# Optimization experiments

Measured on AMD Instinct MI355X. Metric: run time of the kernel, lower is better.

## Reference

```python
import jax, jax.numpy as jnp
import numpy as np

DIM = 512
NUM_HEADS = 8


def setup_inputs() -> dict:
    key = jax.random.key(0)
    ks = jax.random.split(key, 9)
    B, C, H, W = 8, DIM, 32, 32
    s = 1.0 / np.sqrt(DIM)  # conv-style init scale
    return {
        "x": jax.random.normal(ks[0], (B, C, H, W), jnp.float32),
        "Wq": jax.random.normal(ks[1], (DIM, DIM), jnp.float32) * s,
        "bq": jnp.zeros((DIM,), jnp.float32),
        "Wk": jax.random.normal(ks[2], (DIM, DIM), jnp.float32) * s,
        "bk": jnp.zeros((DIM,), jnp.float32),
        "Wv": jax.random.normal(ks[3], (DIM, DIM), jnp.float32) * s,
        "bv": jnp.zeros((DIM,), jnp.float32),
        "Wo": jax.random.normal(ks[4], (DIM, DIM), jnp.float32) * s,
        "bo": jnp.zeros((DIM,), jnp.float32),
    }


def _proj(x, W, b):
    # 1x1 conv == per-pixel linear over channels: [out_c, in_c] x [b, in_c, h, w]
    return jnp.einsum('oc,bchw->bohw', W, x) + b[None, :, None, None]


def reference(x, Wq, bq, Wk, bk, Wv, bv, Wo, bo):
    b, c, h, w = x.shape
    g = NUM_HEADS
    dh = c // g  # per-head channels
    q = _proj(x, Wq, bq)
    k = _proj(x, Wk, bk)
    v = _proj(x, Wv, bv)
    # 'b (g c) h w -> (b g) c (h w)'
    def split_heads(t):
        return t.reshape(b, g, dh, h * w).reshape(b * g, dh, h * w)
    q, k, v = split_heads(q), split_heads(k), split_heads(v)
    # note: scale uses full dim (as in the source), not per-head dim
    a = jnp.einsum('bcs,bct->bst', q, k) / jnp.sqrt(jnp.float32(c))
    a = jax.nn.softmax(a, axis=-1)  # dropout is identity at inference
    o = jnp.einsum('bst,bct->bcs', a, v)  # [(b g), dh, s]
    o = o.reshape(b, g * dh, h, w)  # '(b g) c (h w) -> b (g c) h w'
    return x + _proj(o, Wo, bo)
```

## Files before the change

### kernel.cpp

```cpp
#include <hip/hip_runtime.h>

typedef unsigned short u16;
typedef __attribute__((ext_vector_type(8))) short short8;
typedef __attribute__((ext_vector_type(4))) short sh4;
typedef __attribute__((ext_vector_type(2))) int int2v;
typedef __attribute__((ext_vector_type(4))) float floatx4;

__device__ __forceinline__ float b2f(u16 u) {
  unsigned int x = ((unsigned int)u) << 16;
  return __builtin_bit_cast(float, x);
}
__device__ __forceinline__ u16 f2b(float f) {
  unsigned int x = __builtin_bit_cast(unsigned int, f);
  unsigned int r = (x + 0x7FFFu + ((x >> 16) & 1u)) >> 16;
  return (u16)r;
}
__device__ __forceinline__ unsigned int pk2bf(float a, float b) {
  unsigned int ua = __builtin_bit_cast(unsigned int, a) + 0x8000u;
  unsigned int ub = __builtin_bit_cast(unsigned int, b) + 0x8000u;
  return __builtin_amdgcn_perm(ub, ua, 0x07060302u);
}

#if __has_builtin(__builtin_amdgcn_mfma_f32_16x16x16bf16_1k)
#define MFMA16(a, b, c) __builtin_amdgcn_mfma_f32_16x16x16bf16_1k((a), (b), (c), 0, 0, 0)
#define MFMA16_DRAIN()
#else
__device__ __forceinline__ floatx4 mfma16_fb(sh4 a, sh4 b, floatx4 c) {
  asm volatile("s_nop 1\n\tv_mfma_f32_16x16x16_bf16 %0, %1, %2, %0"
               : "+v"(c) : "v"(a), "v"(b));
  return c;
}
#define MFMA16(a, b, c) mfma16_fb((a), (b), (c))
#define MFMA16_DRAIN() asm volatile("s_nop 7\n\ts_nop 7\n\ts_nop 7")
#endif

#if __has_builtin(__builtin_amdgcn_exp2f)
#define EXP2F(x) __builtin_amdgcn_exp2f(x)
#else
#define EXP2F(x) __expf((x) * 0.6931471805599453f)
#endif

#define MFMA32(a, b, c) __builtin_amdgcn_mfma_f32_16x16x32_bf16((a), (b), (c), 0, 0, 0)

#define GLL16(g, l) __builtin_amdgcn_global_load_lds(                         \
    (const __attribute__((address_space(1))) unsigned int*)(g),               \
    (__attribute__((address_space(3))) unsigned int*)(l), 16, 0, 0)

#define SC_LOG2E 0.06375872f

__device__ __forceinline__ int detect_fp32(const u16* __restrict__ x) {
  __shared__ int cnt;
  if (threadIdx.x == 0) cnt = 0;
  __syncthreads();
  int c = 0;
  if (threadIdx.x < 256) {
#pragma unroll
    for (int i = 0; i < 16; ++i) {
      u16 u = x[threadIdx.x * 16 + i];
      if (((u >> 7) & 0xFF) >= 0xC8) c++;
    }
  }
  if (c) atomicAdd(&cnt, c);
  __syncthreads();
  return cnt > 32;
}

__global__ __launch_bounds__(256) void prep(
    const u16* __restrict__ x,
    const u16* w0, const u16* w1, const u16* w2, const u16* w3,
    const u16* c0, const u16* c1, const u16* c2, const u16* c3,
    u16* __restrict__ xT, u16* __restrict__ Wc, u16* __restrict__ bc, int b0) {
  const int fp32 = detect_fp32(x);
  const int tid = threadIdx.x;
  if (blockIdx.y < 8) {
    __shared__ u16 t[64][65];
    const int lb = blockIdx.z, b = b0 + lb;
    const int p0 = blockIdx.x * 64, cc0 = blockIdx.y * 64;
    const int tx = tid & 63, ty = tid >> 6;
    if (fp32) {
      const float* xb = (const float*)x + (long)b * 524288;
#pragma unroll
      for (int i = 0; i < 16; ++i) {
        int c = ty + i * 4;
        t[c][tx] = f2b(xb[(long)(cc0 + c) * 1024 + p0 + tx]);
      }
    } else {
      const u16* xb = x + (long)b * 524288;
#pragma unroll
      for (int i = 0; i < 16; ++i) {
        int c = ty + i * 4;
        t[c][tx] = xb[(long)(cc0 + c) * 1024 + p0 + tx];
      }
    }
    __syncthreads();
    u16* xTb = xT + (long)lb * 524288;
#pragma unroll
    for (int i = 0; i < 16; ++i) {
      int p = ty + i * 4;
      xTb[(long)(p0 + p) * 512 + cc0 + tx] = t[tx][p];
    }
  } else {
    const u16* srcs[8] = {w0, w1, w2, w3, c0, c1, c2, c3};
    const int nthreads = gridDim.z * 16 * 256;
    const int flat = (blockIdx.z * 16 + blockIdx.x) * 256 + tid;
    for (int vi = flat; vi < 131072; vi += nthreads) {
      int w = vi >> 15;
      int off = (vi & 32767) * 8;
      u16* dst = Wc + w * 262144 + off;
      if (fp32) {
        const float* s = (const float*)srcs[w] + off;
        u16 tmp[8];
#pragma unroll
        for (int r = 0; r < 8; ++r) tmp[r] = f2b(s[r]);
        *(int4*)dst = *(const int4*)tmp;
      } else {
        *(int4*)dst = *(const int4*)(srcs[w] + off);
      }
    }
    for (int gi = flat; gi < 2048; gi += nthreads) {
      int t2 = gi >> 9;
      bc[gi] = fp32 ? f2b(((const float*)srcs[4 + t2])[gi & 511]) : srcs[4 + t2][gi & 511];
    }
  }
}

struct GemmLds {
  u16 As[128][32];
  u16 Bs[128][32];
};

__device__ __forceinline__ void gemm_core(const u16* __restrict__ A, int lda,
                                          const u16* __restrict__ B, int ldb,
                                          int m0, int n0, int K,
                                          GemmLds& lds, floatx4 (&acc)[4][4]) {
  const int tid = threadIdx.x;
  const int wave = tid >> 6, lane = tid & 63;
  const int quad = lane >> 4, l15 = lane & 15;
  const int wm = (wave >> 1) * 64, wn = (wave & 1) * 64;
  const int lrow = lane >> 2, lcol = (lane & 3) * 8;
  for (int k0 = 0; k0 < K; k0 += 32) {
    __syncthreads();
#pragma unroll
    for (int it = 0; it < 2; ++it) {
      const int rbase = wave * 32 + it * 16;
      GLL16(A + (long)(m0 + rbase + lrow) * lda + k0 + lcol, &lds.As[rbase][0]);
      GLL16(B + (long)(n0 + rbase + lrow) * ldb + k0 + lcol, &lds.Bs[rbase][0]);
    }
    __syncthreads();
    short8 af[4], bf[4];
#pragma unroll
    for (int i = 0; i < 4; ++i)
      af[i] = *(const short8*)&lds.As[wm + i * 16 + l15][quad * 8];
#pragma unroll
    for (int j = 0; j < 4; ++j)
      bf[j] = *(const short8*)&lds.Bs[wn + j * 16 + l15][quad * 8];
#pragma unroll
    for (int i = 0; i < 4; ++i)
#pragma unroll
      for (int j = 0; j < 4; ++j)
        acc[i][j] = MFMA32(af[i], bf[j], acc[i][j]);
  }
}

__global__ __launch_bounds__(256) void gemm_qkv(
    const u16* __restrict__ xT, const u16* __restrict__ Wc,
    const u16* __restrict__ bc, u16* __restrict__ Qt, u16* __restrict__ Kt,
    u16* __restrict__ Vv) {
  __shared__ GemmLds lds;
  const long bz = blockIdx.y;
  const u16* xb = xT + bz * 524288;
  const int bx = blockIdx.x;
  const int qk = bx < 64;
  const int t = qk ? bx : bx - 64;
  const int m0 = (t >> 3) * 128, n0 = (t & 7) * 128;
  const u16* A = qk ? xb : (Wc + 524288);
  const u16* B = qk ? Wc : xb;
  floatx4 acc[4][4] = {};
  gemm_core(A, 512, B, 512, m0, n0, 512, lds, acc);
  const int lane = threadIdx.x & 63, wave = threadIdx.x >> 6;
  const int quad = lane >> 4, l15 = lane & 15;
  const int wm = (wave >> 1) * 64, wn = (wave & 1) * 64;
  if (qk) {
    u16* Qz = Qt + bz * 524288;
    u16* Kz = Kt + bz * 524288;
#pragma unroll
    for (int i = 0; i < 4; ++i)
#pragma unroll
      for (int j = 0; j < 4; ++j)
#pragma unroll
        for (int r = 0; r < 4; ++r) {
          int gm = m0 + wm + i * 16 + quad * 4 + r;
          int gn = n0 + wn + j * 16 + l15;
          float v = acc[i][j][r] + b2f(bc[gn]);
          if (gn < 512) Qz[(long)gm * 512 + gn] = f2b(v * SC_LOG2E);
          else Kz[(long)gm * 512 + gn - 512] = f2b(v);
        }
  } else {
    u16* Vz = Vv + bz * 524288;
    const u16* bv = bc + 1024;
#pragma unroll
    for (int i = 0; i < 4; ++i)
#pragma unroll
      for (int j = 0; j < 4; ++j)
#pragma unroll
        for (int r = 0; r < 4; ++r) {
          int gm = m0 + wm + i * 16 + quad * 4 + r;
          int gn = n0 + wn + j * 16 + l15;
          float v = acc[i][j][r] + b2f(bv[gm]);
          Vz[(long)gm * 1024 + gn] = f2b(v);
        }
  }
}

__global__ __launch_bounds__(256) void gemm_out(
    const u16* __restrict__ Wo, const u16* __restrict__ bo,
    const u16* __restrict__ Ow, const u16* __restrict__ xraw,
    u16* __restrict__ out) {
  const int fp32 = detect_fp32(xraw);
  __shared__ GemmLds lds;
  const long bz = blockIdx.z;
  const u16* B = Ow + bz * 524288;
  const int m0 = blockIdx.y * 128, n0 = blockIdx.x * 128;
  floatx4 acc[4][4] = {};
  gemm_core(Wo, 512, B, 512, m0, n0, 512, lds, acc);
  const int lane = threadIdx.x & 63, wave = threadIdx.x >> 6;
  const int quad = lane >> 4, l15 = lane & 15;
  const int wm = (wave >> 1) * 64, wn = (wave & 1) * 64;
#pragma unroll
  for (int i = 0; i < 4; ++i)
#pragma unroll
    for (int j = 0; j < 4; ++j)
#pragma unroll
      for (int r = 0; r < 4; ++r) {
        int gm = m0 + wm + i * 16 + quad * 4 + r;
        int gn = n0 + wn + j * 16 + l15;
        float v = acc[i][j][r] + b2f(bo[gm]);
        long idx = bz * 524288 + (long)gm * 1024 + gn;
        if (fp32) {
          v += ((const float*)xraw)[idx];
          ((float*)out)[idx] = v;
        } else {
          v += b2f(xraw[idx]);
          out[idx] = f2b(v);
        }
      }
}

#define AP 72
__global__ __launch_bounds__(512, 4) void attn(
    const u16* __restrict__ Qt, const u16* __restrict__ Kt,
    const u16* __restrict__ V, u16* __restrict__ O) {
  __shared__ alignas(16) u16 Ks[2][64][AP];
  __shared__ alignas(16) u16 Vs[2][64][AP];
  const int bg = blockIdx.x;
  const int lb = bg >> 3, head = bg & 7;
  const int s0 = blockIdx.y * 128;
  const int tid = threadIdx.x;
  const int wave = tid >> 6, lane = tid & 63;
  const int quad = lane >> 4, l15 = lane & 15;

  const u16* Qb = Qt + (long)lb * 524288 + head * 64;
  const u16* Kb = Kt + (long)lb * 524288 + head * 64;
  const u16* Vb = V + (long)(lb * 512 + head * 64) * 1024;
  u16* Ob = O + (long)lb * 524288 + head * 64;

  short8 bq[2];
#pragma unroll
  for (int kk = 0; kk < 2; ++kk)
    bq[kk] = *(const short8*)&Qb[(long)(s0 + wave * 16 + l15) * 512 +
                                 kk * 32 + quad * 8];

  const int r0 = tid >> 3, o0 = (tid & 7) * 8;
  int4 kreg, vreg;
  kreg = *(const int4*)&Kb[(long)r0 * 512 + o0];
  vreg = *(const int4*)&Vb[(long)r0 * 1024 + o0];
  *(int4*)&Ks[0][r0][o0] = kreg;
  *(int4*)&Vs[0][r0][o0] = vreg;

  floatx4 acc[4] = {};
  floatx4 accl = {};
  const sh4 ones = {(short)0x3F80, (short)0x3F80, (short)0x3F80, (short)0x3F80};

  for (int it16 = 0; it16 < 16; ++it16) {
    const int buf = it16 & 1;
    const int t0n = (it16 + 1) * 64;
    if (it16 < 15) {
      kreg = *(const int4*)&Kb[(long)(t0n + r0) * 512 + o0];
      vreg = *(const int4*)&Vb[(long)r0 * 1024 + t0n + o0];
    }
    __syncthreads();

    floatx4 p[4] = {};
#pragma unroll
    for (int kk = 0; kk < 2; ++kk) {
      short8 ak[4];
#pragma unroll
      for (int mi = 0; mi < 4; ++mi)
        ak[mi] = *(const short8*)&Ks[buf][mi * 16 + l15][kk * 32 + quad * 8];
#pragma unroll
      for (int mi = 0; mi < 4; ++mi)
        p[mi] = MFMA32(ak[mi], bq[kk], p[mi]);
    }

    sh4 pk[4];
#pragma unroll
    for (int mi = 0; mi < 4; ++mi) {
      float e0 = EXP2F(p[mi][0]);
      float e1 = EXP2F(p[mi][1]);
      float e2 = EXP2F(p[mi][2]);
      float e3 = EXP2F(p[mi][3]);
      int2v w;
      w.x = (int)pk2bf(e0, e1);
      w.y = (int)pk2bf(e2, e3);
      pk[mi] = __builtin_bit_cast(sh4, w);
    }

#pragma unroll
    for (int mi = 0; mi < 4; ++mi) accl = MFMA16(ones, pk[mi], accl);

#pragma unroll
    for (int mi = 0; mi < 4; ++mi) {
      sh4 av[4];
#pragma unroll
      for (int ci = 0; ci < 4; ++ci)
        av[ci] = *(const sh4*)&Vs[buf][ci * 16 + l15][mi * 16 + quad * 4];
#pragma unroll
      for (int ci = 0; ci < 4; ++ci)
        acc[ci] = MFMA16(av[ci], pk[mi], acc[ci]);
    }

    if (it16 < 15) {
      const int nb = 1 - buf;
      *(int4*)&Ks[nb][r0][o0] = kreg;
      *(int4*)&Vs[nb][r0][o0] = vreg;
    }
  }
  MFMA16_DRAIN();

  const float inv = 1.0f / accl[0];

  u16 (*Os)[AP] = (u16(*)[AP]) & Ks[0][0][0];
  __syncthreads();
#pragma unroll
  for (int ci = 0; ci < 4; ++ci) {
    int2v w;
    w.x = (int)pk2bf(acc[ci][0] * inv, acc[ci][1] * inv);
    w.y = (int)pk2bf(acc[ci][2] * inv, acc[ci][3] * inv);
    *(int2v*)&Os[wave * 16 + l15][ci * 16 + quad * 4] = w;
  }
  __syncthreads();
  {
    const int srow = tid >> 2, c16 = (tid & 3) * 16;
    *(int4*)&Ob[(long)(s0 + srow) * 512 + c16] = *(const int4*)&Os[srow][c16];
    *(int4*)&Ob[(long)(s0 + srow) * 512 + c16 + 8] = *(const int4*)&Os[srow][c16 + 8];
  }
}

extern "C" void kernel_launch(void* const* d_in, const int* in_sizes, int n_in,
                              void* d_out, int out_size, void* d_ws, size_t ws_size,
                              hipStream_t stream) {
  const u16* x  = (const u16*)d_in[0];
  const u16* Wq = (const u16*)d_in[1];
  const u16* bq = (const u16*)d_in[2];
  const u16* Wk = (const u16*)d_in[3];
  const u16* bk = (const u16*)d_in[4];
  const u16* Wv = (const u16*)d_in[5];
  const u16* bv = (const u16*)d_in[6];
  const u16* Wo = (const u16*)d_in[7];
  const u16* bo = (const u16*)d_in[8];
  u16* out = (u16*)d_out;
  u16* ws = (u16*)d_ws;

  const size_t PLAN_A_BYTES = 27267072;

  if (ws_size >= PLAN_A_BYTES) {
    u16* xT = ws;
    u16* Kt = ws + 4194304;
    u16* Vv = ws + 8388608;
    u16* Wc = ws + 12582912;
    u16* bc = ws + 13631488;
    u16* Qt = out;
    u16* Ow = xT;

    prep<<<dim3(16, 9, 8), 256, 0, stream>>>(x, Wq, Wk, Wv, Wo,
                                             bq, bk, bv, bo, xT, Wc, bc, 0);
    gemm_qkv<<<dim3(96, 8), 256, 0, stream>>>(xT, Wc, bc, Qt, Kt, Vv);
    attn<<<dim3(64, 8), 512, 0, stream>>>(Qt, Kt, Vv, Ow);
    gemm_out<<<dim3(8, 4, 8), 256, 0, stream>>>(Wc + 786432, bc + 1536, Ow, x, out);
  } else {
    u16* Ow = ws;
    u16* Kt = ws + 4194304;
    u16* Vv = ws + 6291456;
    u16* Wc = ws + 8388608;
    u16* bc = ws + 9437184;
    u16* Qt = out;

    for (int phase = 0; phase < 2; ++phase) {
      const int b0 = phase * 4;
      u16* xT = Ow + (long)phase * 2097152;
      prep<<<dim3(16, 9, 4), 256, 0, stream>>>(x, Wq, Wk, Wv, Wo,
                                               bq, bk, bv, bo, xT, Wc, bc, b0);
      gemm_qkv<<<dim3(96, 4), 256, 0, stream>>>(xT, Wc, bc, Qt, Kt, Vv);
      attn<<<dim3(32, 8), 512, 0, stream>>>(Qt, Kt, Vv, Ow + (long)b0 * 524288);
    }
    gemm_out<<<dim3(8, 4, 8), 256, 0, stream>>>(Wc + 786432, bc + 1536, Ow, x, out);
  }
}
```

Before: 177.2 us.

## Fuse prep, QKV, attention and output GEMM into one persistent kernel with grid barriers

Replaces four separate kernel launches with a single persistent kernel of 512 blocks that runs the stages back to back, separated by atomic-counter grid barriers. The GEMM tiles are reshaped to K-step 64 with 8 waves, and the output GEMM uses 128x64 tiles so each block gets one job. The aim is to remove launch overhead and per-kernel tail idle time. The grid barrier relies on all 512 blocks being co-resident, which deadlocks if occupancy is insufficient. It also drops the small-workspace fallback path.

```diff
diff --git a/kernel.cpp b/kernel.cpp
--- a/kernel.cpp
+++ b/kernel.cpp
@@ -47,6 +47,26 @@
     (__attribute__((address_space(3))) unsigned int*)(l), 16, 0, 0)
 
 #define SC_LOG2E 0.06375872f
+#define NB 512
+#define AP 72
+
+union SMem {
+  struct { u16 t[2][64][65]; } tr;
+  struct { u16 As[128][64]; u16 Bs[128][64]; } gm;
+  struct { u16 Ks[2][64][AP]; u16 Vs[2][64][AP]; } at;
+};
+
+__device__ __forceinline__ void gbar(unsigned* cnt, unsigned target) {
+  __syncthreads();
+  if (threadIdx.x == 0) {
+    __threadfence();
+    __hip_atomic_fetch_add(cnt, 1u, __ATOMIC_RELAXED, __HIP_MEMORY_SCOPE_AGENT);
+    while (__hip_atomic_load(cnt, __ATOMIC_RELAXED, __HIP_MEMORY_SCOPE_AGENT) < target)
+      __builtin_amdgcn_s_sleep(2);
+    __threadfence();
+  }
+  __syncthreads();
+}
 
 __device__ __forceinline__ int detect_fp32(const u16* __restrict__ x) {
   __shared__ int cnt;
@@ -65,47 +85,165 @@
   return cnt > 32;
 }
 
-__global__ __launch_bounds__(256) void prep(
+__device__ __forceinline__ void gemm_128x128(const u16* __restrict__ A,
+                                             const u16* __restrict__ B,
+                                             SMem& sm, floatx4 (&acc)[4][2]) {
+  const int tid = threadIdx.x;
+  const int wave = tid >> 6, lane = tid & 63;
+  const int quad = lane >> 4, l15 = lane & 15;
+  const int wm = (wave >> 2) * 64, wn = (wave & 3) * 32;
+  const int srow = lane >> 3, sseg = (lane & 7) * 8;
+  for (int k0 = 0; k0 < 512; k0 += 64) {
+    __syncthreads();
+#pragma unroll
+    for (int r = 0; r < 2; ++r) {
+      const int ch = wave + r * 8;
+      GLL16(A + (long)(ch * 8 + srow) * 512 + k0 + sseg, &sm.gm.As[ch * 8][0]);
+      GLL16(B + (long)(ch * 8 + srow) * 512 + k0 + sseg, &sm.gm.Bs[ch * 8][0]);
+    }
+    __syncthreads();
+#pragma unroll
+    for (int kk = 0; kk < 2; ++kk) {
+      short8 af[4], bf[2];
+#pragma unroll
+      for (int i = 0; i < 4; ++i)
+        af[i] = *(const short8*)&sm.gm.As[wm + i * 16 + l15][kk * 32 + quad * 8];
+#pragma unroll
+      for (int j = 0; j < 2; ++j)
+        bf[j] = *(const short8*)&sm.gm.Bs[wn + j * 16 + l15][kk * 32 + quad * 8];
+#pragma unroll
+      for (int i = 0; i < 4; ++i)
+#pragma unroll
+        for (int j = 0; j < 2; ++j)
+          acc[i][j] = MFMA32(af[i], bf[j], acc[i][j]);
+    }
+  }
+}
+
+__device__ __forceinline__ void gemm_128x64(const u16* __restrict__ A,
+                                            const u16* __restrict__ B,
+                                            SMem& sm, floatx4 (&acc)[2][2]) {
+  const int tid = threadIdx.x;
+  const int wave = tid >> 6, lane = tid & 63;
+  const int quad = lane >> 4, l15 = lane & 15;
+  const int wm = (wave >> 1) * 32, wn = (wave & 1) * 32;
+  const int srow = lane >> 3, sseg = (lane & 7) * 8;
+  for (int k0 = 0; k0 < 512; k0 += 64) {
+    __syncthreads();
+#pragma unroll
+    for (int r = 0; r < 3; ++r) {
+      const int ch = wave + r * 8;
+      if (ch < 16)
+        GLL16(A + (long)(ch * 8 + srow) * 512 + k0 + sseg, &sm.gm.As[ch * 8][0]);
+      else
+        GLL16(B + (long)((ch - 16) * 8 + srow) * 512 + k0 + sseg,
+              &sm.gm.Bs[(ch - 16) * 8][0]);
+    }
+    __syncthreads();
+#pragma unroll
+    for (int kk = 0; kk < 2; ++kk) {
+      short8 af[2], bf[2];
+#pragma unroll
+      for (int i = 0; i < 2; ++i)
+        af[i] = *(const short8*)&sm.gm.As[wm + i * 16 + l15][kk * 32 + quad * 8];
+#pragma unroll
+      for (int j = 0; j < 2; ++j)
+        bf[j] = *(const short8*)&sm.gm.Bs[wn + j * 16 + l15][kk * 32 + quad * 8];
+#pragma unroll
+      for (int i = 0; i < 2; ++i)
+#pragma unroll
+        for (int j = 0; j < 2; ++j)
+          acc[i][j] = MFMA32(af[i], bf[j], acc[i][j]);
+    }
+  }
+}
+
+__device__ __forceinline__ void qkv_job(int j, const u16* __restrict__ xT,
+                                        const u16* __restrict__ Wc,
+                                        const u16* __restrict__ bc,
+                                        u16* __restrict__ Qt, u16* __restrict__ Kt,
+                                        u16* __restrict__ Vv, SMem& sm) {
+  const int lane = threadIdx.x & 63, wave = threadIdx.x >> 6;
+  const int quad = lane >> 4, l15 = lane & 15;
+  const int wm = (wave >> 2) * 64, wn = (wave & 3) * 32;
+  floatx4 acc[4][2] = {};
+  if (j < 512) {
+    const int jm = j >> 3, jn = j & 7;
+    const int b = jm >> 3, mrow = (jm & 7) * 128;
+    gemm_128x128(xT + (long)b * 524288 + (long)mrow * 512, Wc + (long)jn * 65536,
+                 sm, acc);
+    u16* Qz = Qt + (long)b * 524288;
+    u16* Kz = Kt + (long)b * 524288;
+    const int gnb = jn * 128 + wn;
+#pragma unroll
+    for (int i = 0; i < 4; ++i)
+#pragma unroll
+      for (int j2 = 0; j2 < 2; ++j2)
+#pragma unroll
+        for (int r = 0; r < 4; ++r) {
+          int gm = mrow + wm + i * 16 + quad * 4 + r;
+          int gn = gnb + j2 * 16 + l15;
+          float v = acc[i][j2][r] + b2f(bc[gn]);
+          if (gn < 512) Qz[(long)gm * 512 + gn] = f2b(v * SC_LOG2E);
+          else Kz[(long)gm * 512 + gn - 512] = f2b(v);
+        }
+  } else {
+    const int vj = j - 512;
+    const int b = vj >> 5, t = vj & 31;
+    const int m0 = (t >> 3) * 128, n0 = (t & 7) * 128;
+    gemm_128x128(Wc + 524288 + (long)m0 * 512, xT + (long)b * 524288 + (long)n0 * 512,
+                 sm, acc);
+    u16* Vz = Vv + (long)b * 524288;
+#pragma unroll
+    for (int i = 0; i < 4; ++i)
+#pragma unroll
+      for (int j2 = 0; j2 < 2; ++j2)
+#pragma unroll
+        for (int r = 0; r < 4; ++r) {
+          int gm = m0 + wm + i * 16 + quad * 4 + r;
+          int gn = n0 + wn + j2 * 16 + l15;
+          Vz[(long)gm * 1024 + gn] = f2b(acc[i][j2][r] + b2f(bc[1024 + gm]));
+        }
+  }
+}
+
+__global__ __launch_bounds__(512, 4) void fused(
     const u16* __restrict__ x,
     const u16* w0, const u16* w1, const u16* w2, const u16* w3,
     const u16* c0, const u16* c1, const u16* c2, const u16* c3,
-    u16* __restrict__ xT, u16* __restrict__ Wc, u16* __restrict__ bc, int b0) {
+    u16* __restrict__ xT, u16* __restrict__ Kt, u16* __restrict__ Vv,
+    u16* __restrict__ Wc, u16* __restrict__ bc,
+    u16* __restrict__ Qt, u16* __restrict__ outp, unsigned* __restrict__ bar) {
+  __shared__ SMem sm;
+  const int bid = blockIdx.x, tid = threadIdx.x;
   const int fp32 = detect_fp32(x);
-  const int tid = threadIdx.x;
-  if (blockIdx.y < 8) {
-    __shared__ u16 t[64][65];
-    const int lb = blockIdx.z, b = b0 + lb;
-    const int p0 = blockIdx.x * 64, cc0 = blockIdx.y * 64;
-    const int tx = tid & 63, ty = tid >> 6;
+  u16* Ow = xT;
+
+  {
+    const int sub = tid >> 8, st = tid & 255;
+    const int tj = bid * 2 + sub;
+    const int b = tj >> 7, rem = tj & 127;
+    const int p0 = (rem >> 3) * 64, cc0 = (rem & 7) * 64;
+    const int tx = st & 63, ty = st >> 6;
     if (fp32) {
       const float* xb = (const float*)x + (long)b * 524288;
 #pragma unroll
       for (int i = 0; i < 16; ++i) {
         int c = ty + i * 4;
-        t[c][tx] = f2b(xb[(long)(cc0 + c) * 1024 + p0 + tx]);
+        sm.tr.t[sub][c][tx] = f2b(xb[(long)(cc0 + c) * 1024 + p0 + tx]);
       }
     } else {
       const u16* xb = x + (long)b * 524288;
 #pragma unroll
       for (int i = 0; i < 16; ++i) {
         int c = ty + i * 4;
-        t[c][tx] = xb[(long)(cc0 + c) * 1024 + p0 + tx];
-      }
-    }
-    __syncthreads();
-    u16* xTb = xT + (long)lb * 524288;
-#pragma unroll
-    for (int i = 0; i < 16; ++i) {
-      int p = ty + i * 4;
-      xTb[(long)(p0 + p) * 512 + cc0 + tx] = t[tx][p];
-    }
-  } else {
+        sm.tr.t[sub][c][tx] = xb[(long)(cc0 + c) * 1024 + p0 + tx];
+      }
+    }
     const u16* srcs[8] = {w0, w1, w2, w3, c0, c1, c2, c3};
-    const int nthreads = gridDim.z * 16 * 256;
-    const int flat = (blockIdx.z * 16 + blockIdx.x) * 256 + tid;
-    for (int vi = flat; vi < 131072; vi += nthreads) {
-      int w = vi >> 15;
-      int off = (vi & 32767) * 8;
+    const int flat = bid * 512 + tid;
+    if (flat < 131072) {
+      int w = flat >> 15, off = (flat & 32767) * 8;
       u16* dst = Wc + w * 262144 + off;
       if (fp32) {
         const float* s = (const float*)srcs[w] + off;
@@ -117,242 +255,153 @@
         *(int4*)dst = *(const int4*)(srcs[w] + off);
       }
     }
-    for (int gi = flat; gi < 2048; gi += nthreads) {
-      int t2 = gi >> 9;
-      bc[gi] = fp32 ? f2b(((const float*)srcs[4 + t2])[gi & 511]) : srcs[4 + t2][gi & 511];
-    }
-  }
-}
-
-struct GemmLds {
-  u16 As[128][32];
-  u16 Bs[128][32];
-};
-
-__device__ __forceinline__ void gemm_core(const u16* __restrict__ A, int lda,
-                                          const u16* __restrict__ B, int ldb,
-                                          int m0, int n0, int K,
-                                          GemmLds& lds, floatx4 (&acc)[4][4]) {
-  const int tid = threadIdx.x;
-  const int wave = tid >> 6, lane = tid & 63;
-  const int quad = lane >> 4, l15 = lane & 15;
-  const int wm = (wave >> 1) * 64, wn = (wave & 1) * 64;
-  const int lrow = lane >> 2, lcol = (lane & 3) * 8;
-  for (int k0 = 0; k0 < K; k0 += 32) {
-    __syncthreads();
-#pragma unroll
-    for (int it = 0; it < 2; ++it) {
-      const int rbase = wave * 32 + it * 16;
-      GLL16(A + (long)(m0 + rbase + lrow) * lda + k0 + lcol, &lds.As[rbase][0]);
-      GLL16(B + (long)(n0 + rbase + lrow) * ldb + k0 + lcol, &lds.Bs[rbase][0]);
-    }
-    __syncthreads();
-    short8 af[4], bf[4];
-#pragma unroll
-    for (int i = 0; i < 4; ++i)
-      af[i] = *(const short8*)&lds.As[wm + i * 16 + l15][quad * 8];
-#pragma unroll
-    for (int j = 0; j < 4; ++j)
-      bf[j] = *(const short8*)&lds.Bs[wn + j * 16 + l15][quad * 8];
-#pragma unroll
-    for (int i = 0; i < 4; ++i)
-#pragma unroll
-      for (int j = 0; j < 4; ++j)
-        acc[i][j] = MFMA32(af[i], bf[j], acc[i][j]);
-  }
-}
-
-__global__ __launch_bounds__(256) void gemm_qkv(
-    const u16* __restrict__ xT, const u16* __restrict__ Wc,
-    const u16* __restrict__ bc, u16* __restrict__ Qt, u16* __restrict__ Kt,
-    u16* __restrict__ Vv) {
-  __shared__ GemmLds lds;
-  const long bz = blockIdx.y;
-  const u16* xb = xT + bz * 524288;
-  const int bx = blockIdx.x;
-  const int qk = bx < 64;
-  const int t = qk ? bx : bx - 64;
-  const int m0 = (t >> 3) * 128, n0 = (t & 7) * 128;
-  const u16* A = qk ? xb : (Wc + 524288);
-  const u16* B = qk ? Wc : xb;
-  floatx4 acc[4][4] = {};
-  gemm_core(A, 512, B, 512, m0, n0, 512, lds, acc);
-  const int lane = threadIdx.x & 63, wave = threadIdx.x >> 6;
-  const int quad = lane >> 4, l15 = lane & 15;
-  const int wm = (wave >> 1) * 64, wn = (wave & 1) * 64;
-  if (qk) {
-    u16* Qz = Qt + bz * 524288;
-    u16* Kz = Kt + bz * 524288;
-#pragma unroll
-    for (int i = 0; i < 4; ++i)
-#pragma unroll
-      for (int j = 0; j < 4; ++j)
+    if (flat < 2048) {
+      int t2 = flat >> 9;
+      bc[flat] = fp32 ? f2b(((const float*)srcs[4 + t2])[flat & 511])
+                      : srcs[4 + t2][flat & 511];
+    }
+    __syncthreads();
+    u16* xTb = xT + (long)b * 524288;
+#pragma unroll
+    for (int i = 0; i < 16; ++i) {
+      int p = ty + i * 4;
+      xTb[(long)(p0 + p) * 512 + cc0 + tx] = sm.tr.t[sub][tx][p];
+    }
+  }
+  gbar(bar, NB);
+
+  qkv_job(bid, xT, Wc, bc, Qt, Kt, Vv, sm);
+  if (bid < 256) qkv_job(bid + 512, xT, Wc, bc, Qt, Kt, Vv, sm);
+  gbar(bar, 2 * NB);
+
+  {
+    const int bg = bid & 63, lb = bg >> 3, head = bg & 7;
+    const int s0 = (bid >> 6) * 128;
+    const int wave = tid >> 6, lane = tid & 63;
+    const int quad = lane >> 4, l15 = lane & 15;
+    const u16* Qb = Qt + (long)lb * 524288 + head * 64;
+    const u16* Kb = Kt + (long)lb * 524288 + head * 64;
+    const u16* Vb = Vv + (long)(lb * 512 + head * 64) * 1024;
+    u16* Ob = Ow + (long)lb * 524288 + head * 64;
+
+    short8 bq[2];
+#pragma unroll
+    for (int kk = 0; kk < 2; ++kk)
+      bq[kk] = *(const short8*)&Qb[(long)(s0 + wave * 16 + l15) * 512 +
+                                   kk * 32 + quad * 8];
+
+    const int r0 = tid >> 3, o0 = (tid & 7) * 8;
+    int4 kreg = *(const int4*)&Kb[(long)r0 * 512 + o0];
+    int4 vreg = *(const int4*)&Vb[(long)r0 * 1024 + o0];
+    *(int4*)&sm.at.Ks[0][r0][o0] = kreg;
+    *(int4*)&sm.at.Vs[0][r0][o0] = vreg;
+
+    floatx4 acc[4] = {};
+    floatx4 accl = {};
+    const sh4 ones = {(short)0x3F80, (short)0x3F80, (short)0x3F80, (short)0x3F80};
+
+    for (int it16 = 0; it16 < 16; ++it16) {
+      const int buf = it16 & 1;
+      const int t0n = (it16 + 1) * 64;
+      if (it16 < 15) {
+        kreg = *(const int4*)&Kb[(long)(t0n + r0) * 512 + o0];
+        vreg = *(const int4*)&Vb[(long)r0 * 1024 + t0n + o0];
+      }
+      __syncthreads();
+
+      floatx4 p[4] = {};
+#pragma unroll
+      for (int kk = 0; kk < 2; ++kk) {
+        short8 ak[4];
+#pragma unroll
+        for (int mi = 0; mi < 4; ++mi)
+          ak[mi] = *(const short8*)&sm.at.Ks[buf][mi * 16 + l15][kk * 32 + quad * 8];
+#pragma unroll
+        for (int mi = 0; mi < 4; ++mi)
+          p[mi] = MFMA32(ak[mi], bq[kk], p[mi]);
+      }
+
+      sh4 pk[4];
+#pragma unroll
+      for (int mi = 0; mi < 4; ++mi) {
+        float e0 = EXP2F(p[mi][0]);
+        float e1 = EXP2F(p[mi][1]);
+        float e2 = EXP2F(p[mi][2]);
+        float e3 = EXP2F(p[mi][3]);
+        int2v w;
+        w.x = (int)pk2bf(e0, e1);
+        w.y = (int)pk2bf(e2, e3);
+        pk[mi] = __builtin_bit_cast(sh4, w);
+      }
+
+#pragma unroll
+      for (int mi = 0; mi < 4; ++mi) accl = MFMA16(ones, pk[mi], accl);
+
+#pragma unroll
+      for (int mi = 0; mi < 4; ++mi) {
+        sh4 av[4];
+#pragma unroll
+        for (int ci = 0; ci < 4; ++ci)
+          av[ci] = *(const sh4*)&sm.at.Vs[buf][ci * 16 + l15][mi * 16 + quad * 4];
+#pragma unroll
+        for (int ci = 0; ci < 4; ++ci)
+          acc[ci] = MFMA16(av[ci], pk[mi], acc[ci]);
+      }
+
+      if (it16 < 15) {
+        const int nb = 1 - buf;
+        *(int4*)&sm.at.Ks[nb][r0][o0] = kreg;
+        *(int4*)&sm.at.Vs[nb][r0][o0] = vreg;
+      }
+    }
+    MFMA16_DRAIN();
+
+    const float inv = 1.0f / accl[0];
+    u16 (*Os)[AP] = (u16(*)[AP]) & sm.at.Ks[0][0][0];
+    __syncthreads();
+#pragma unroll
+    for (int ci = 0; ci < 4; ++ci) {
+      int2v w;
+      w.x = (int)pk2bf(acc[ci][0] * inv, acc[ci][1] * inv);
+      w.y = (int)pk2bf(acc[ci][2] * inv, acc[ci][3] * inv);
+      *(int2v*)&Os[wave * 16 + l15][ci * 16 + quad * 4] = w;
+    }
+    __syncthreads();
+    {
+      const int srow = tid >> 2, c16 = (tid & 3) * 16;
+      *(int4*)&Ob[(long)(s0 + srow) * 512 + c16] = *(const int4*)&Os[srow][c16];
+      *(int4*)&Ob[(long)(s0 + srow) * 512 + c16 + 8] = *(const int4*)&Os[srow][c16 + 8];
+    }
+  }
+  gbar(bar, 3 * NB);
+
+  {
+    const int b = bid >> 6, t = bid & 63;
+    const int m0 = (t >> 4) * 128, n0 = (t & 15) * 64;
+    floatx4 acc[2][2] = {};
+    gemm_128x64(Wc + 786432 + (long)m0 * 512, Ow + (long)b * 524288 + (long)n0 * 512,
+                sm, acc);
+    const int lane = tid & 63, wave = tid >> 6;
+    const int quad = lane >> 4, l15 = lane & 15;
+    const int wm = (wave >> 1) * 32, wn = (wave & 1) * 32;
+#pragma unroll
+    for (int i = 0; i < 2; ++i)
+#pragma unroll
+      for (int j2 = 0; j2 < 2; ++j2)
 #pragma unroll
         for (int r = 0; r < 4; ++r) {
           int gm = m0 + wm + i * 16 + quad * 4 + r;
-          int gn = n0 + wn + j * 16 + l15;
-          float v = acc[i][j][r] + b2f(bc[gn]);
-          if (gn < 512) Qz[(long)gm * 512 + gn] = f2b(v * SC_LOG2E);
-          else Kz[(long)gm * 512 + gn - 512] = f2b(v);
+          int gn = n0 + wn + j2 * 16 + l15;
+          float v = acc[i][j2][r] + b2f(bc[1536 + gm]);
+          long idx = (long)b * 524288 + (long)gm * 1024 + gn;
+          if (fp32) {
+            v += ((const float*)x)[idx];
+            ((float*)outp)[idx] = v;
+          } else {
+            v += b2f(x[idx]);
+            outp[idx] = f2b(v);
+          }
         }
-  } else {
-    u16* Vz = Vv + bz * 524288;
-    const u16* bv = bc + 1024;
-#pragma unroll
-    for (int i = 0; i < 4; ++i)
-#pragma unroll
-      for (int j = 0; j < 4; ++j)
-#pragma unroll
-        for (int r = 0; r < 4; ++r) {
-          int gm = m0 + wm + i * 16 + quad * 4 + r;
-          int gn = n0 + wn + j * 16 + l15;
-          float v = acc[i][j][r] + b2f(bv[gm]);
-          Vz[(long)gm * 1024 + gn] = f2b(v);
-        }
-  }
-}
-
-__global__ __launch_bounds__(256) void gemm_out(
-    const u16* __restrict__ Wo, const u16* __restrict__ bo,
-    const u16* __restrict__ Ow, const u16* __restrict__ xraw,
-    u16* __restrict__ out) {
-  const int fp32 = detect_fp32(xraw);
-  __shared__ GemmLds lds;
-  const long bz = blockIdx.z;
-  const u16* B = Ow + bz * 524288;
-  const int m0 = blockIdx.y * 128, n0 = blockIdx.x * 128;
-  floatx4 acc[4][4] = {};
-  gemm_core(Wo, 512, B, 512, m0, n0, 512, lds, acc);
-  const int lane = threadIdx.x & 63, wave = threadIdx.x >> 6;
-  const int quad = lane >> 4, l15 = lane & 15;
-  const int wm = (wave >> 1) * 64, wn = (wave & 1) * 64;
-#pragma unroll
-  for (int i = 0; i < 4; ++i)
-#pragma unroll
-    for (int j = 0; j < 4; ++j)
-#pragma unroll
-      for (int r = 0; r < 4; ++r) {
-        int gm = m0 + wm + i * 16 + quad * 4 + r;
-        int gn = n0 + wn + j * 16 + l15;
-        float v = acc[i][j][r] + b2f(bo[gm]);
-        long idx = bz * 524288 + (long)gm * 1024 + gn;
-        if (fp32) {
-          v += ((const float*)xraw)[idx];
-          ((float*)out)[idx] = v;
-        } else {
-          v += b2f(xraw[idx]);
-          out[idx] = f2b(v);
-        }
-      }
-}
-
-#define AP 72
-__global__ __launch_bounds__(512, 4) void attn(
-    const u16* __restrict__ Qt, const u16* __restrict__ Kt,
-    const u16* __restrict__ V, u16* __restrict__ O) {
-  __shared__ alignas(16) u16 Ks[2][64][AP];
-  __shared__ alignas(16) u16 Vs[2][64][AP];
-  const int bg = blockIdx.x;
-  const int lb = bg >> 3, head = bg & 7;
-  const int s0 = blockIdx.y * 128;
-  const int tid = threadIdx.x;
-  const int wave = tid >> 6, lane = tid & 63;
-  const int quad = lane >> 4, l15 = lane & 15;
-
-  const u16* Qb = Qt + (long)lb * 524288 + head * 64;
-  const u16* Kb = Kt + (long)lb * 524288 + head * 64;
-  const u16* Vb = V + (long)(lb * 512 + head * 64) * 1024;
-  u16* Ob = O + (long)lb * 524288 + head * 64;
-
-  short8 bq[2];
-#pragma unroll
-  for (int kk = 0; kk < 2; ++kk)
-    bq[kk] = *(const short8*)&Qb[(long)(s0 + wave * 16 + l15) * 512 +
-                                 kk * 32 + quad * 8];
-
-  const int r0 = tid >> 3, o0 = (tid & 7) * 8;
-  int4 kreg, vreg;
-  kreg = *(const int4*)&Kb[(long)r0 * 512 + o0];
-  vreg = *(const int4*)&Vb[(long)r0 * 1024 + o0];
-  *(int4*)&Ks[0][r0][o0] = kreg;
-  *(int4*)&Vs[0][r0][o0] = vreg;
-
-  floatx4 acc[4] = {};
-  floatx4 accl = {};
-  const sh4 ones = {(short)0x3F80, (short)0x3F80, (short)0x3F80, (short)0x3F80};
-
-  for (int it16 = 0; it16 < 16; ++it16) {
-    const int buf = it16 & 1;
-    const int t0n = (it16 + 1) * 64;
-    if (it16 < 15) {
-      kreg = *(const int4*)&Kb[(long)(t0n + r0) * 512 + o0];
-      vreg = *(const int4*)&Vb[(long)r0 * 1024 + t0n + o0];
-    }
-    __syncthreads();
-
-    floatx4 p[4] = {};
-#pragma unroll
-    for (int kk = 0; kk < 2; ++kk) {
-      short8 ak[4];
-#pragma unroll
-      for (int mi = 0; mi < 4; ++mi)
-        ak[mi] = *(const short8*)&Ks[buf][mi * 16 + l15][kk * 32 + quad * 8];
-#pragma unroll
-      for (int mi = 0; mi < 4; ++mi)
-        p[mi] = MFMA32(ak[mi], bq[kk], p[mi]);
-    }
-
-    sh4 pk[4];
-#pragma unroll
-    for (int mi = 0; mi < 4; ++mi) {
-      float e0 = EXP2F(p[mi][0]);
-      float e1 = EXP2F(p[mi][1]);
-      float e2 = EXP2F(p[mi][2]);
-      float e3 = EXP2F(p[mi][3]);
-      int2v w;
-      w.x = (int)pk2bf(e0, e1);
-      w.y = (int)pk2bf(e2, e3);
-      pk[mi] = __builtin_bit_cast(sh4, w);
-    }
-
-#pragma unroll
-    for (int mi = 0; mi < 4; ++mi) accl = MFMA16(ones, pk[mi], accl);
-
-#pragma unroll
-    for (int mi = 0; mi < 4; ++mi) {
-      sh4 av[4];
-#pragma unroll
-      for (int ci = 0; ci < 4; ++ci)
-        av[ci] = *(const sh4*)&Vs[buf][ci * 16 + l15][mi * 16 + quad * 4];
-#pragma unroll
-      for (int ci = 0; ci < 4; ++ci)
-        acc[ci] = MFMA16(av[ci], pk[mi], acc[ci]);
-    }
-
-    if (it16 < 15) {
-      const int nb = 1 - buf;
-      *(int4*)&Ks[nb][r0][o0] = kreg;
-      *(int4*)&Vs[nb][r0][o0] = vreg;
-    }
-  }
-  MFMA16_DRAIN();
-
-  const float inv = 1.0f / accl[0];
-
-  u16 (*Os)[AP] = (u16(*)[AP]) & Ks[0][0][0];
-  __syncthreads();
-#pragma unroll
-  for (int ci = 0; ci < 4; ++ci) {
-    int2v w;
-    w.x = (int)pk2bf(acc[ci][0] * inv, acc[ci][1] * inv);
-    w.y = (int)pk2bf(acc[ci][2] * inv, acc[ci][3] * inv);
-    *(int2v*)&Os[wave * 16 + l15][ci * 16 + quad * 4] = w;
-  }
-  __syncthreads();
-  {
-    const int srow = tid >> 2, c16 = (tid & 3) * 16;
-    *(int4*)&Ob[(long)(s0 + srow) * 512 + c16] = *(const int4*)&Os[srow][c16];
-    *(int4*)&Ob[(long)(s0 + srow) * 512 + c16 + 8] = *(const int4*)&Os[srow][c16 + 8];
   }
 }
 
@@ -368,41 +417,17 @@
   const u16* bv = (const u16*)d_in[6];
   const u16* Wo = (const u16*)d_in[7];
   const u16* bo = (const u16*)d_in[8];
-  u16* out = (u16*)d_out;
   u16* ws = (u16*)d_ws;
 
-  const size_t PLAN_A_BYTES = 27267072;
-
-  if (ws_size >= PLAN_A_BYTES) {
-    u16* xT = ws;
-    u16* Kt = ws + 4194304;
-    u16* Vv = ws + 8388608;
-    u16* Wc = ws + 12582912;
-    u16* bc = ws + 13631488;
-    u16* Qt = out;
-    u16* Ow = xT;
-
-    prep<<<dim3(16, 9, 8), 256, 0, stream>>>(x, Wq, Wk, Wv, Wo,
-                                             bq, bk, bv, bo, xT, Wc, bc, 0);
-    gemm_qkv<<<dim3(96, 8), 256, 0, stream>>>(xT, Wc, bc, Qt, Kt, Vv);
-    attn<<<dim3(64, 8), 512, 0, stream>>>(Qt, Kt, Vv, Ow);
-    gemm_out<<<dim3(8, 4, 8), 256, 0, stream>>>(Wc + 786432, bc + 1536, Ow, x, out);
-  } else {
-    u16* Ow = ws;
-    u16* Kt = ws + 4194304;
-    u16* Vv = ws + 6291456;
-    u16* Wc = ws + 8388608;
-    u16* bc = ws + 9437184;
-    u16* Qt = out;
-
-    for (int phase = 0; phase < 2; ++phase) {
-      const int b0 = phase * 4;
-      u16* xT = Ow + (long)phase * 2097152;
-      prep<<<dim3(16, 9, 4), 256, 0, stream>>>(x, Wq, Wk, Wv, Wo,
-                                               bq, bk, bv, bo, xT, Wc, bc, b0);
-      gemm_qkv<<<dim3(96, 4), 256, 0, stream>>>(xT, Wc, bc, Qt, Kt, Vv);
-      attn<<<dim3(32, 8), 512, 0, stream>>>(Qt, Kt, Vv, Ow + (long)b0 * 524288);
-    }
-    gemm_out<<<dim3(8, 4, 8), 256, 0, stream>>>(Wc + 786432, bc + 1536, Ow, x, out);
-  }
-}
+  u16* xT = ws;
+  u16* Kt = ws + 4194304;
+  u16* Vv = ws + 8388608;
+  u16* Wc = ws + 12582912;
+  u16* bc = ws + 13631488;
+  unsigned* bar = (unsigned*)(ws + 13633536);
+  u16* Qt = (u16*)d_out;
+
+  hipMemsetAsync(bar, 0, 128, stream);
+  fused<<<NB, 512, 0, stream>>>(x, Wq, Wk, Wv, Wo, bq, bk, bv, bo,
+                                xT, Kt, Vv, Wc, bc, Qt, (u16*)d_out, bar);
+}
```

New measurement: 326.3 us. 84.1% more time.
